# Kernel tuning notes

Measured on AMD Instinct MI355X. Metric: run time of the kernel, lower is better.

The kernel has to match this reference:

```python
import jax, jax.numpy as jnp
import numpy as np
from jax import lax


def _conv(x, w, b):
    # x: [B, Cin, H, W], w: [Cout, Cin, 3, 3] -> [B, Cout, H, W] (SAME padding)
    y = lax.conv_general_dilated(x, w, (1, 1), 'SAME',
                                 dimension_numbers=('NCHW', 'OIHW', 'NCHW'))
    return y + b[None, :, None, None]


def _cell_step(h, c, x, w, b):
    gates = _conv(jnp.concatenate([x, h], axis=1), w, b)  # [B, 4, H, W]
    i, f, o, g = jnp.split(gates, 4, axis=1)
    c = jax.nn.sigmoid(f) * c + jax.nn.sigmoid(i) * jnp.tanh(g)
    h = jax.nn.sigmoid(o) * jnp.tanh(c)
    return h, c


def setup_inputs() -> dict:
    key = jax.random.key(0)
    k1, k2, k3 = jax.random.split(key, 3)
    T, B, C, H, W = 20, 1, 1, 1024, 1024
    data = jax.random.normal(k1, (T, B, C, H, W), dtype=jnp.float32)
    enc_w = jax.random.normal(k2, (4, 2, 3, 3), dtype=jnp.float32) * 0.3
    enc_b = jnp.zeros((4,), dtype=jnp.float32)
    dec_w = jax.random.normal(k3, (4, 2, 3, 3), dtype=jnp.float32) * 0.3
    dec_b = jnp.zeros((4,), dtype=jnp.float32)
    return {"data": data, "enc_w": enc_w, "enc_b": enc_b,
            "dec_w": dec_w, "dec_b": dec_b,
            "epoch": 0, "T_en": 20, "T_de": 20}


def reference(data, enc_w, enc_b, dec_w, dec_b, epoch, T_en, T_de):
    B, C, H, W = data.shape[1:]
    h0 = jnp.zeros((B, C, H, W), dtype=data.dtype)
    c0 = jnp.zeros((B, C, H, W), dtype=data.dtype)

    def enc_step(carry, x):
        h, c = _cell_step(carry[0], carry[1], x, enc_w, enc_b)
        return (h, c), None

    (h_enc, _), _ = lax.scan(enc_step, (h0, c0), data[epoch:T_en])

    # decoder_input = encoder_h[0][:, None, :, :] -> with B=C=1 this is h_enc itself
    dec_in = h_enc[0][:, None, :, :]  # [1, 1, H, W]

    def dec_step(carry, _):
        h, c = _cell_step(carry[0], carry[1], dec_in, dec_w, dec_b)
        return (h, c), None

    (h_dec, _), _ = lax.scan(dec_step, (h0, c0), None, length=T_de)
    return h_dec[0, 0]  # [H, W]
```

## Files before the change

kernel.cpp:

```cpp
#include <hip/hip_runtime.h>

#define W 1024
#define H 1024
#define PADX 16
#define PADY 8
#define XS 1056
#define YS 1040
#define FR ((size_t)XS * (size_t)YS)
#define NPIX (H * W)
#define TROWS 32
#define TCOLS 64
#define LRN 48
#define LCV 96
#define LCW 100
#define NSLOT 460
#define NB 512

typedef float v2f __attribute__((ext_vector_type(2)));

__device__ __forceinline__ float frcp_(float v) { return __builtin_amdgcn_rcpf(v); }
__device__ __forceinline__ float sigm_(float v) { return frcp_(1.0f + __expf(-v)); }
__device__ __forceinline__ float tanh_(float v) {
    return 1.0f - 2.0f * frcp_(1.0f + __expf(2.0f * v));
}

__global__ __launch_bounds__(256) void init_pad(const float* __restrict__ data,
                                                float* __restrict__ ws) {
    const int R4 = XS / 4;
    const size_t n4_fr  = 20 * (FR / 4);
    const size_t n4_tot = 26 * (FR / 4);
    size_t i = (size_t)blockIdx.x * blockDim.x + threadIdx.x;
    const size_t stride = (size_t)gridDim.x * blockDim.x;
    float4* w4 = (float4*)ws;
    for (; i < n4_tot; i += stride) {
        float4 v = make_float4(0.f, 0.f, 0.f, 0.f);
        if (i < n4_fr) {
            size_t f = i / (size_t)(YS * R4);
            int rem = (int)(i - f * (size_t)(YS * R4));
            int pr  = rem / R4;
            int k4  = rem - pr * R4;
            if (pr >= PADY && pr < PADY + H &&
                k4 >= PADX / 4 && k4 < PADX / 4 + W / 4) {
                v = *(const float4*)(data + f * (size_t)NPIX +
                                     (size_t)(pr - PADY) * W + (4 * k4 - PADX));
            }
        }
        w4[i] = v;
    }
}

__device__ __forceinline__ void conv3x8_pk(const float* __restrict__ p, int stride,
                                           const float* __restrict__ wg, int wofs,
                                           v2f acc[4][4]) {
#pragma unroll
    for (int dy = 0; dy < 3; ++dy) {
        const float4 A  = *(const float4*)p;
        const float4 Bq = *(const float4*)(p + 4);
        const float lm = p[-1], rp = p[8];
        const v2f E0 = {A.x, A.y},  E1 = {A.z, A.w};
        const v2f E2 = {Bq.x, Bq.y}, E3 = {Bq.z, Bq.w};
        const v2f O0 = {lm, A.x},   O1 = {A.y, A.z};
        const v2f O2 = {A.w, Bq.x}, O3 = {Bq.y, Bq.z}, O4 = {Bq.w, rp};
#pragma unroll
        for (int co = 0; co < 4; ++co) {
            const float w0 = wg[co * 18 + wofs + dy * 3 + 0];
            const float w1 = wg[co * 18 + wofs + dy * 3 + 1];
            const float w2 = wg[co * 18 + wofs + dy * 3 + 2];
            const v2f W0 = {w0, w0}, W1 = {w1, w1}, W2 = {w2, w2};
            acc[co][0] += W0 * O0 + W1 * E0 + W2 * O1;
            acc[co][1] += W0 * O1 + W1 * E1 + W2 * O2;
            acc[co][2] += W0 * O2 + W1 * E2 + W2 * O3;
            acc[co][3] += W0 * O3 + W1 * E3 + W2 * O4;
        }
        p += stride;
    }
}

template<int NSTEPS, bool XCONST>
__global__ __launch_bounds__(NB, 4) void fusedN(
    const float* __restrict__ xbase, size_t xstep,
    const float* __restrict__ hin, const float* __restrict__ cin,
    float* __restrict__ hout, float* __restrict__ cout_,
    const float* __restrict__ wg, const float* __restrict__ bg,
    float* __restrict__ dout, int zero_init)
{
    __shared__ float hT[2][LRN * LCW];
    const int tid = threadIdx.x;
    const int c0 = (blockIdx.x & 15) * TCOLS;
    const int r0 = (blockIdx.x >> 4) * TROWS;

    const bool has = tid < NSLOT;
    const int q   = tid / 10;
    const int jj  = tid - q * 10;
    const int lr  = 1 + q;
    const int lc  = 8 + 8 * jj;
    const int gr  = r0 - 8 + lr;
    const int gc0 = c0 - 8 + 8 * jj;
    const size_t gofs = (size_t)(gr + PADY) * XS + (gc0 + PADX);
    const bool inimg = ((unsigned)gr < (unsigned)H) && ((unsigned)gc0 < (unsigned)W);

    for (int idx = tid; idx < LRN * (LCV / 4); idx += NB) {
        const int r = idx / (LCV / 4);
        const int k = idx - r * (LCV / 4);
        float4 v = make_float4(0.f, 0.f, 0.f, 0.f);
        if (!zero_init)
            v = *(const float4*)(hin + (size_t)(r0 + r) * XS + (c0 + 4 * k));
        *(float4*)(&hT[0][r * LCW + 4 * k]) = v;
        *(float4*)(&hT[1][r * LCW + 4 * k]) = make_float4(0.f, 0.f, 0.f, 0.f);
    }

    float cc[8];
    if (has && !zero_init) {
        const float4 a = *(const float4*)(cin + gofs);
        const float4 b = *(const float4*)(cin + gofs + 4);
        cc[0] = a.x; cc[1] = a.y; cc[2] = a.z; cc[3] = a.w;
        cc[4] = b.x; cc[5] = b.y; cc[6] = b.z; cc[7] = b.w;
    } else {
#pragma unroll
        for (int e = 0; e < 8; ++e) cc[e] = 0.f;
    }

    v2f xacc[4][4];
    if constexpr (XCONST) {
        if (has) {
#pragma unroll
            for (int co = 0; co < 4; ++co) {
                const v2f bb = {bg[co], bg[co]};
#pragma unroll
                for (int j = 0; j < 4; ++j) xacc[co][j] = bb;
            }
            conv3x8_pk(xbase + gofs - XS, XS, wg, 0, xacc);
        }
    }
    __syncthreads();

    float hh[8];
#pragma unroll
    for (int e = 0; e < 8; ++e) hh[e] = 0.f;

#pragma unroll
    for (int i = 1; i <= NSTEPS; ++i) {
        const float* hR = hT[(i + 1) & 1];
        float* hW       = hT[i & 1];
        const bool act = has && (lr >= i) && (lr < LRN - i);
        if (act) {
            v2f acc[4][4];
            if constexpr (XCONST) {
#pragma unroll
                for (int co = 0; co < 4; ++co)
#pragma unroll
                    for (int j = 0; j < 4; ++j) acc[co][j] = xacc[co][j];
            } else {
#pragma unroll
                for (int co = 0; co < 4; ++co) {
                    const v2f bb = {bg[co], bg[co]};
#pragma unroll
                    for (int j = 0; j < 4; ++j) acc[co][j] = bb;
                }
                conv3x8_pk(xbase + (size_t)(i - 1) * xstep + gofs - XS, XS,
                           wg, 0, acc);
            }
            conv3x8_pk(hR + (lr - 1) * LCW + lc, LCW, wg, 9, acc);
#pragma unroll
            for (int jp = 0; jp < 4; ++jp) {
#pragma unroll
                for (int s = 0; s < 2; ++s) {
                    const int e = 2 * jp + s;
                    const float gi = sigm_(acc[0][jp][s]);
                    const float gf = sigm_(acc[1][jp][s]);
                    const float go = sigm_(acc[2][jp][s]);
                    const float gg = tanh_(acc[3][jp][s]);
                    const float cn = gf * cc[e] + gi * gg;
                    cc[e] = cn;
                    hh[e] = inimg ? (go * tanh_(cn)) : 0.f;
                }
            }
            *(float4*)(hW + lr * LCW + lc)     = make_float4(hh[0], hh[1], hh[2], hh[3]);
            *(float4*)(hW + lr * LCW + lc + 4) = make_float4(hh[4], hh[5], hh[6], hh[7]);
        }
        __syncthreads();
    }

    if (has && lr >= 8 && lr < 8 + TROWS && jj >= 1 && jj <= 8) {
        if (dout) {
            const size_t o = (size_t)gr * W + gc0;
            *(float4*)(dout + o)     = make_float4(hh[0], hh[1], hh[2], hh[3]);
            *(float4*)(dout + o + 4) = make_float4(hh[4], hh[5], hh[6], hh[7]);
        } else {
            *(float4*)(hout + gofs)      = make_float4(hh[0], hh[1], hh[2], hh[3]);
            *(float4*)(hout + gofs + 4)  = make_float4(hh[4], hh[5], hh[6], hh[7]);
            *(float4*)(cout_ + gofs)     = make_float4(cc[0], cc[1], cc[2], cc[3]);
            *(float4*)(cout_ + gofs + 4) = make_float4(cc[4], cc[5], cc[6], cc[7]);
        }
    }
}

extern "C" void kernel_launch(void* const* d_in, const int* in_sizes, int n_in,
                              void* d_out, int out_size, void* d_ws, size_t ws_size,
                              hipStream_t stream) {
    const float* data  = (const float*)d_in[0];
    const float* enc_w = (const float*)d_in[1];
    const float* enc_b = (const float*)d_in[2];
    const float* dec_w = (const float*)d_in[3];
    const float* dec_b = (const float*)d_in[4];

    float* ws   = (float*)d_ws;
    float* xpad = ws;
    float* hE0  = ws + 20 * FR;
    float* hE1  = ws + 21 * FR;
    float* cE0  = ws + 22 * FR;
    float* cE1  = ws + 23 * FR;
    float* hX   = ws + 24 * FR;
    float* cX   = ws + 25 * FR;
    float* dout = (float*)d_out;

    init_pad<<<2048, 256, 0, stream>>>(data, ws);

    dim3 blk(NB), grd(512);
    fusedN<8, false><<<grd, blk, 0, stream>>>(xpad,           FR, nullptr, nullptr,
                                              hE1, cE1, enc_w, enc_b, nullptr, 1);
    fusedN<8, false><<<grd, blk, 0, stream>>>(xpad +  8 * FR, FR, hE1, cE1,
                                              hE0, cE0, enc_w, enc_b, nullptr, 0);
    fusedN<4, false><<<grd, blk, 0, stream>>>(xpad + 16 * FR, FR, hE0, cE0,
                                              hE1, cE1, enc_w, enc_b, nullptr, 0);
    fusedN<8, true><<<grd, blk, 0, stream>>>(hE1, 0, nullptr, nullptr,
                                             hE0, cE0, dec_w, dec_b, nullptr, 1);
    fusedN<8, true><<<grd, blk, 0, stream>>>(hE1, 0, hE0, cE0,
                                             hX,  cX,  dec_w, dec_b, nullptr, 0);
    fusedN<4, true><<<grd, blk, 0, stream>>>(hE1, 0, hX,  cX,
                                             nullptr, nullptr, dec_w, dec_b, dout, 0);
}
```

Before: 376.4 us.

## Read input frames directly with edge-guarded loads and prescale gate weights for exp2

Drops the padded copy of all 20 input frames. The encoder kernels now read the raw data tensor directly: interior tiles take an unguarded fast path, and border tiles use a bounds-checked load path. The init kernel now only zeroes the six padded state buffers, which removes a large read-and-write pass over the workspace. It also stores copies of the weights and biases prescaled by log2(e) (and by 2·log2(e) for the tanh gate), so the gate nonlinearities use exp2 directly and skip a multiply each. The launch-bounds hint is switched to an explicit waves-per-EU attribute. The cost is extra branching on edge tiles and uncached reads from the unpadded frames.

```diff
diff --git a/kernel.cpp b/kernel.cpp
--- a/kernel.cpp
+++ b/kernel.cpp
@@ -15,37 +15,55 @@
 #define LCW 100
 #define NSLOT 460
 #define NB 512
+#define LOG2E 1.4426950408889634f
+#define TWOL  2.8853900817779268f
 
 typedef float v2f __attribute__((ext_vector_type(2)));
 
 __device__ __forceinline__ float frcp_(float v) { return __builtin_amdgcn_rcpf(v); }
-__device__ __forceinline__ float sigm_(float v) { return frcp_(1.0f + __expf(-v)); }
-__device__ __forceinline__ float tanh_(float v) {
-    return 1.0f - 2.0f * frcp_(1.0f + __expf(2.0f * v));
-}
-
-__global__ __launch_bounds__(256) void init_pad(const float* __restrict__ data,
-                                                float* __restrict__ ws) {
-    const int R4 = XS / 4;
-    const size_t n4_fr  = 20 * (FR / 4);
-    const size_t n4_tot = 26 * (FR / 4);
+__device__ __forceinline__ float exp2_(float v) { return __builtin_amdgcn_exp2f(v); }
+__device__ __forceinline__ float sigm2_(float v)  { return frcp_(1.0f + exp2_(-v)); }
+__device__ __forceinline__ float tanhg2_(float v) { return 1.0f - 2.0f * frcp_(1.0f + exp2_(v)); }
+__device__ __forceinline__ float tanhc_(float v)  { return 1.0f - 2.0f * frcp_(1.0f + exp2_(TWOL * v)); }
+
+__global__ __launch_bounds__(256) void init_ws(const float* __restrict__ ew,
+                                               const float* __restrict__ eb,
+                                               const float* __restrict__ dw,
+                                               const float* __restrict__ db,
+                                               float* __restrict__ ws) {
+    const size_t n4 = 6 * (FR / 4);
     size_t i = (size_t)blockIdx.x * blockDim.x + threadIdx.x;
     const size_t stride = (size_t)gridDim.x * blockDim.x;
     float4* w4 = (float4*)ws;
-    for (; i < n4_tot; i += stride) {
-        float4 v = make_float4(0.f, 0.f, 0.f, 0.f);
-        if (i < n4_fr) {
-            size_t f = i / (size_t)(YS * R4);
-            int rem = (int)(i - f * (size_t)(YS * R4));
-            int pr  = rem / R4;
-            int k4  = rem - pr * R4;
-            if (pr >= PADY && pr < PADY + H &&
-                k4 >= PADX / 4 && k4 < PADX / 4 + W / 4) {
-                v = *(const float4*)(data + f * (size_t)NPIX +
-                                     (size_t)(pr - PADY) * W + (4 * k4 - PADX));
-            }
-        }
-        w4[i] = v;
+    const float4 z = make_float4(0.f, 0.f, 0.f, 0.f);
+    for (; i < n4; i += stride) w4[i] = z;
+    if (blockIdx.x == 0) {
+        float* wsc = ws + 6 * FR;
+        const int t = threadIdx.x;
+        if (t < 72)                   wsc[t] = ew[t] * ((t / 18 == 3) ? TWOL : LOG2E);
+        else if (t < 76)              wsc[t] = eb[t - 72] * ((t - 72 == 3) ? TWOL : LOG2E);
+        else if (t >= 80 && t < 152)  wsc[t] = dw[t - 80] * (((t - 80) / 18 == 3) ? TWOL : LOG2E);
+        else if (t >= 152 && t < 156) wsc[t] = db[t - 152] * ((t - 152 == 3) ? TWOL : LOG2E);
+    }
+}
+
+__device__ __forceinline__ void acc_row(float4 A, float4 Bq, float lm, float rp,
+                                        const float* __restrict__ wg, int wofs, int dy,
+                                        v2f acc[4][4]) {
+    const v2f E0 = {A.x, A.y},   E1 = {A.z, A.w};
+    const v2f E2 = {Bq.x, Bq.y}, E3 = {Bq.z, Bq.w};
+    const v2f O0 = {lm, A.x},    O1 = {A.y, A.z};
+    const v2f O2 = {A.w, Bq.x},  O3 = {Bq.y, Bq.z}, O4 = {Bq.w, rp};
+#pragma unroll
+    for (int co = 0; co < 4; ++co) {
+        const float w0 = wg[co * 18 + wofs + dy * 3 + 0];
+        const float w1 = wg[co * 18 + wofs + dy * 3 + 1];
+        const float w2 = wg[co * 18 + wofs + dy * 3 + 2];
+        const v2f W0 = {w0, w0}, W1 = {w1, w1}, W2 = {w2, w2};
+        acc[co][0] += W0 * O0 + W1 * E0 + W2 * O1;
+        acc[co][1] += W0 * O1 + W1 * E1 + W2 * O2;
+        acc[co][2] += W0 * O2 + W1 * E2 + W2 * O3;
+        acc[co][3] += W0 * O3 + W1 * E3 + W2 * O4;
     }
 }
 
@@ -54,35 +72,42 @@
                                            v2f acc[4][4]) {
 #pragma unroll
     for (int dy = 0; dy < 3; ++dy) {
-        const float4 A  = *(const float4*)p;
-        const float4 Bq = *(const float4*)(p + 4);
-        const float lm = p[-1], rp = p[8];
-        const v2f E0 = {A.x, A.y},  E1 = {A.z, A.w};
-        const v2f E2 = {Bq.x, Bq.y}, E3 = {Bq.z, Bq.w};
-        const v2f O0 = {lm, A.x},   O1 = {A.y, A.z};
-        const v2f O2 = {A.w, Bq.x}, O3 = {Bq.y, Bq.z}, O4 = {Bq.w, rp};
-#pragma unroll
-        for (int co = 0; co < 4; ++co) {
-            const float w0 = wg[co * 18 + wofs + dy * 3 + 0];
-            const float w1 = wg[co * 18 + wofs + dy * 3 + 1];
-            const float w2 = wg[co * 18 + wofs + dy * 3 + 2];
-            const v2f W0 = {w0, w0}, W1 = {w1, w1}, W2 = {w2, w2};
-            acc[co][0] += W0 * O0 + W1 * E0 + W2 * O1;
-            acc[co][1] += W0 * O1 + W1 * E1 + W2 * O2;
-            acc[co][2] += W0 * O2 + W1 * E2 + W2 * O3;
-            acc[co][3] += W0 * O3 + W1 * E3 + W2 * O4;
-        }
+        acc_row(*(const float4*)p, *(const float4*)(p + 4), p[-1], p[8], wg, wofs, dy, acc);
         p += stride;
     }
 }
 
-template<int NSTEPS, bool XCONST>
-__global__ __launch_bounds__(NB, 4) void fusedN(
-    const float* __restrict__ xbase, size_t xstep,
-    const float* __restrict__ hin, const float* __restrict__ cin,
-    float* __restrict__ hout, float* __restrict__ cout_,
-    const float* __restrict__ wg, const float* __restrict__ bg,
-    float* __restrict__ dout, int zero_init)
+__device__ __forceinline__ void conv3x8_edge(const float* __restrict__ base, int gr, int gc0,
+                                             const float* __restrict__ wg, int wofs,
+                                             v2f acc[4][4]) {
+    const bool colA = (unsigned)gc0 < (unsigned)W;
+    const bool lmok = (unsigned)(gc0 - 1) < (unsigned)W;
+    const bool rpok = (unsigned)(gc0 + 8) < (unsigned)W;
+#pragma unroll
+    for (int dy = 0; dy < 3; ++dy) {
+        const int ry = gr - 1 + dy;
+        const bool rok = (unsigned)ry < (unsigned)H;
+        const float* row = base + (long)ry * W;
+        float4 A = make_float4(0.f, 0.f, 0.f, 0.f);
+        float4 Bq = make_float4(0.f, 0.f, 0.f, 0.f);
+        float lm = 0.f, rp = 0.f;
+        if (rok) {
+            if (colA) { A = *(const float4*)(row + gc0); Bq = *(const float4*)(row + gc0 + 4); }
+            if (lmok) lm = row[gc0 - 1];
+            if (rpok) rp = row[gc0 + 8];
+        }
+        acc_row(A, Bq, lm, rp, wg, wofs, dy, acc);
+    }
+}
+
+template<int NSTEPS, bool XC>
+__global__ __launch_bounds__(NB)
+__attribute__((amdgpu_waves_per_eu(4, 4)))
+void fusedN(const float* __restrict__ xbase, size_t xstep,
+            const float* __restrict__ hin, const float* __restrict__ cin,
+            float* __restrict__ hout, float* __restrict__ cout_,
+            const float* __restrict__ wg, const float* __restrict__ bg,
+            float* __restrict__ dout, int zero_init)
 {
     __shared__ float hT[2][LRN * LCW];
     const int tid = threadIdx.x;
@@ -98,6 +123,7 @@
     const int gc0 = c0 - 8 + 8 * jj;
     const size_t gofs = (size_t)(gr + PADY) * XS + (gc0 + PADX);
     const bool inimg = ((unsigned)gr < (unsigned)H) && ((unsigned)gc0 < (unsigned)W);
+    const bool safe = (r0 >= 8) && (r0 + 40 <= H) && (c0 >= 16) && (c0 + 80 <= W);
 
     for (int idx = tid; idx < LRN * (LCV / 4); idx += NB) {
         const int r = idx / (LCV / 4);
@@ -121,7 +147,7 @@
     }
 
     v2f xacc[4][4];
-    if constexpr (XCONST) {
+    if constexpr (XC) {
         if (has) {
 #pragma unroll
             for (int co = 0; co < 4; ++co) {
@@ -145,7 +171,7 @@
         const bool act = has && (lr >= i) && (lr < LRN - i);
         if (act) {
             v2f acc[4][4];
-            if constexpr (XCONST) {
+            if constexpr (XC) {
 #pragma unroll
                 for (int co = 0; co < 4; ++co)
 #pragma unroll
@@ -157,8 +183,11 @@
 #pragma unroll
                     for (int j = 0; j < 4; ++j) acc[co][j] = bb;
                 }
-                conv3x8_pk(xbase + (size_t)(i - 1) * xstep + gofs - XS, XS,
-                           wg, 0, acc);
+                const float* xp = xbase + (size_t)(i - 1) * xstep;
+                if (safe)
+                    conv3x8_pk(xp + (size_t)(gr - 1) * W + gc0, W, wg, 0, acc);
+                else
+                    conv3x8_edge(xp, gr, gc0, wg, 0, acc);
             }
             conv3x8_pk(hR + (lr - 1) * LCW + lc, LCW, wg, 9, acc);
 #pragma unroll
@@ -166,13 +195,13 @@
 #pragma unroll
                 for (int s = 0; s < 2; ++s) {
                     const int e = 2 * jp + s;
-                    const float gi = sigm_(acc[0][jp][s]);
-                    const float gf = sigm_(acc[1][jp][s]);
-                    const float go = sigm_(acc[2][jp][s]);
-                    const float gg = tanh_(acc[3][jp][s]);
+                    const float gi = sigm2_(acc[0][jp][s]);
+                    const float gf = sigm2_(acc[1][jp][s]);
+                    const float go = sigm2_(acc[2][jp][s]);
+                    const float gg = tanhg2_(acc[3][jp][s]);
                     const float cn = gf * cc[e] + gi * gg;
                     cc[e] = cn;
-                    hh[e] = inimg ? (go * tanh_(cn)) : 0.f;
+                    hh[e] = inimg ? (go * tanhc_(cn)) : 0.f;
                 }
             }
             *(float4*)(hW + lr * LCW + lc)     = make_float4(hh[0], hh[1], hh[2], hh[3]);
@@ -204,29 +233,33 @@
     const float* dec_w = (const float*)d_in[3];
     const float* dec_b = (const float*)d_in[4];
 
-    float* ws   = (float*)d_ws;
-    float* xpad = ws;
-    float* hE0  = ws + 20 * FR;
-    float* hE1  = ws + 21 * FR;
-    float* cE0  = ws + 22 * FR;
-    float* cE1  = ws + 23 * FR;
-    float* hX   = ws + 24 * FR;
-    float* cX   = ws + 25 * FR;
+    float* ws  = (float*)d_ws;
+    float* hE1 = ws + 0 * FR;
+    float* cE1 = ws + 1 * FR;
+    float* hE0 = ws + 2 * FR;
+    float* cE0 = ws + 3 * FR;
+    float* hX  = ws + 4 * FR;
+    float* cX  = ws + 5 * FR;
+    float* wsc = ws + 6 * FR;
+    const float* encW = wsc;
+    const float* encB = wsc + 72;
+    const float* decW = wsc + 80;
+    const float* decB = wsc + 152;
     float* dout = (float*)d_out;
 
-    init_pad<<<2048, 256, 0, stream>>>(data, ws);
+    init_ws<<<2048, 256, 0, stream>>>(enc_w, enc_b, dec_w, dec_b, ws);
 
     dim3 blk(NB), grd(512);
-    fusedN<8, false><<<grd, blk, 0, stream>>>(xpad,           FR, nullptr, nullptr,
-                                              hE1, cE1, enc_w, enc_b, nullptr, 1);
-    fusedN<8, false><<<grd, blk, 0, stream>>>(xpad +  8 * FR, FR, hE1, cE1,
-                                              hE0, cE0, enc_w, enc_b, nullptr, 0);
-    fusedN<4, false><<<grd, blk, 0, stream>>>(xpad + 16 * FR, FR, hE0, cE0,
-                                              hE1, cE1, enc_w, enc_b, nullptr, 0);
+    fusedN<8, false><<<grd, blk, 0, stream>>>(data,                    (size_t)NPIX,
+                                              nullptr, nullptr, hE1, cE1, encW, encB, nullptr, 1);
+    fusedN<8, false><<<grd, blk, 0, stream>>>(data + (size_t)8 * NPIX, (size_t)NPIX,
+                                              hE1, cE1, hE0, cE0, encW, encB, nullptr, 0);
+    fusedN<4, false><<<grd, blk, 0, stream>>>(data + (size_t)16 * NPIX, (size_t)NPIX,
+                                              hE0, cE0, hE1, cE1, encW, encB, nullptr, 0);
     fusedN<8, true><<<grd, blk, 0, stream>>>(hE1, 0, nullptr, nullptr,
-                                             hE0, cE0, dec_w, dec_b, nullptr, 1);
+                                             hE0, cE0, decW, decB, nullptr, 1);
     fusedN<8, true><<<grd, blk, 0, stream>>>(hE1, 0, hE0, cE0,
-                                             hX,  cX,  dec_w, dec_b, nullptr, 0);
+                                             hX,  cX,  decW, decB, nullptr, 0);
     fusedN<4, true><<<grd, blk, 0, stream>>>(hE1, 0, hX,  cX,
-                                             nullptr, nullptr, dec_w, dec_b, dout, 0);
-}
+                                             nullptr, nullptr, decW, decB, dout, 0);
+}
```

After: 350.2 us. -7.0%, faster.
